# Kernel optimization log

Hardware: AMD Instinct MI355X
Metric: run time of the kernel (lower is better)

## Reference

```python
import jax, jax.numpy as jnp
from jax import lax
import numpy as np

B, C, L, H, W = 2, 64, 16, 64, 64
K = 7
NG = 4  # GroupNorm groups (SpatialGroupNorm(4, channels))


def setup_inputs() -> dict:
    key = jax.random.key(0)
    ks = jax.random.split(key, 16)
    s = lambda i, shape, sc: jax.random.normal(ks[i], shape, jnp.float32) * sc
    return {
        "x": s(0, (B, C, L, H, W), 1.0),
        "dt": jax.random.uniform(ks[1], (B, L), jnp.float32, 0.1, 1.0),
        "W_sp": s(2, (C, C, K, K), 0.02),      # spatial 7x7 conv (OIHW)
        "W_dc": s(3, (C, C), 0.1),             # 1x1x1 depth conv
        "b_dc": jnp.zeros((C,), jnp.float32),
        "gn_g": jnp.ones((C,), jnp.float32),
        "gn_b": jnp.zeros((C,), jnp.float32),
        "W_in": s(4, (2 * C, C), 0.1),         # pw_conv_in 1x1 -> 2C (gated)
        "b_in": jnp.zeros((2 * C,), jnp.float32),
        "W_out": s(5, (C, C), 0.1),            # pw_conv_out 1x1
        "b_out": jnp.zeros((C,), jnp.float32),
        "nu_log": s(6, (C,), 0.5),             # LRU log decay rate
        "theta_log": s(7, (C,), 0.5),          # LRU log frequency
        "c_re": s(8, (C,), 0.5),               # LRU output mix (real)
        "c_im": s(9, (C,), 0.5),               # LRU output mix (imag)
        "d_skip": s(10, (C,), 0.5),            # LRU feedthrough
    }


def reference(x, dt, W_sp, W_dc, b_dc, gn_g, gn_b, W_in, b_in, W_out, b_out,
              nu_log, theta_log, c_re, c_im, d_skip):
    Bb, Cc, Ll, Hh, Ww = x.shape
    pad = W_sp.shape[-1] // 2
    # --- GatedConvBlock: FactorizedPeriodicConv3d (per-frame 2D conv) ---
    xf = x.transpose(0, 2, 1, 3, 4).reshape(Bb * Ll, Cc, Hh, Ww)  # [B*L,C,H,W]
    xp = jnp.pad(xf, ((0, 0), (0, 0), (0, 0), (pad, pad)), mode='wrap')    # circular W
    xp = jnp.pad(xp, ((0, 0), (0, 0), (pad, pad), (0, 0)), mode='edge')    # replicate H
    y = lax.conv_general_dilated(xp, W_sp, (1, 1), 'VALID',
                                 dimension_numbers=('NCHW', 'OIHW', 'NCHW'))
    y = jnp.einsum('nchw,oc->nohw', y, W_dc) + b_dc[None, :, None, None]   # depth 1x1x1
    # --- SpatialGroupNorm (per frame, 4 groups) ---
    g = y.reshape(Bb * Ll, NG, Cc // NG, Hh, Ww)
    mu = g.mean(axis=(2, 3, 4), keepdims=True)
    var = g.var(axis=(2, 3, 4), keepdims=True)
    y = ((g - mu) * lax.rsqrt(var + 1e-5)).reshape(Bb * Ll, Cc, Hh, Ww)
    y = y * gn_g[None, :, None, None] + gn_b[None, :, None, None]
    # --- gated pointwise convs + residual ---
    h = jnp.einsum('nchw,oc->nohw', y, W_in) + b_in[None, :, None, None]
    x1, x2 = jnp.split(h, 2, axis=1)
    z = x1 * jax.nn.sigmoid(x2)
    z = jnp.einsum('nchw,oc->nohw', z, W_out) + b_out[None, :, None, None]
    u = xf + z                                     # residual, [B*L,C,H,W]
    u = u.reshape(Bb, Ll, Cc, Hh, Ww).transpose(1, 0, 2, 3, 4)  # [L,B,C,H,W]
    # --- LRU: dt-dependent complex diagonal recurrence over L ---
    decay = jnp.exp(-jnp.exp(nu_log)[None, None, :] * dt[:, :, None])   # [B,L,C]
    phase = jnp.exp(theta_log)[None, None, :] * dt[:, :, None]          # [B,L,C]
    lam_re = (decay * jnp.cos(phase)).transpose(1, 0, 2)[..., None, None]  # [L,B,C,1,1]
    lam_im = (decay * jnp.sin(phase)).transpose(1, 0, 2)[..., None, None]
    gamma = jnp.sqrt(jnp.maximum(1.0 - decay ** 2, 1e-6)).transpose(1, 0, 2)[..., None, None]
    cr = c_re[None, :, None, None]
    ci = c_im[None, :, None, None]
    ds = d_skip[None, :, None, None]

    def step(carry, inputs):
        h_re, h_im = carry
        ut, lr, li, gm = inputs
        nr = lr * h_re - li * h_im + gm * ut
        ni = li * h_re + lr * h_im
        yt = cr * nr + ci * ni + ds * ut
        return (nr, ni), yt

    init = (jnp.zeros((Bb, Cc, Hh, Ww), x.dtype), jnp.zeros((Bb, Cc, Hh, Ww), x.dtype))
    _, ys = lax.scan(step, init, (u, lam_re, lam_im, gamma))   # ys: [L,B,C,H,W]
    return ys.transpose(1, 2, 0, 3, 4)                         # [B,C,L,H,W]
```

## Files before the change

### kernel.cpp

```cpp
#include <hip/hip_runtime.h>
#include <hip/hip_bf16.h>

typedef short bf16x8 __attribute__((ext_vector_type(8)));
typedef float f32x16 __attribute__((ext_vector_type(16)));

#define B_ 2
#define C_ 64
#define L_ 16
#define N_ 32
#define HW_ 4096

#define BY_WPH  0u
#define BY_WP1  401408u
#define BY_WP2  434176u
#define BY_OFF1 450560u
#define BY_LR   451072u
#define BY_LI   459264u
#define BY_GM   467456u
#define BY_PART 475648u
#define BY_XHI  524288u
#define BY_U    524288u

__device__ __forceinline__ unsigned short f2bf(float v) {
    unsigned int u = __float_as_uint(v);
    unsigned int r = u + 0x7FFFu + ((u >> 16) & 1u);
    return (unsigned short)(r >> 16);
}
__device__ __forceinline__ float bf2f(unsigned short s) {
    return __uint_as_float(((unsigned int)s) << 16);
}

__global__ void k_setup(const float* __restrict__ W_sp, const float* __restrict__ W_dc,
                        unsigned short* __restrict__ WpH,
                        const float* __restrict__ W_in, const float* __restrict__ b_in,
                        const float* __restrict__ W_out,
                        const float* __restrict__ gn_g, const float* __restrict__ gn_b,
                        unsigned short* __restrict__ WP1, unsigned short* __restrict__ WP2,
                        float* __restrict__ OFF1,
                        const float* __restrict__ dt, const float* __restrict__ nu_log,
                        const float* __restrict__ theta_log,
                        float* __restrict__ lr_t, float* __restrict__ li_t,
                        float* __restrict__ gm_t) {
    int blk = blockIdx.x, tid = threadIdx.x;
    if (blk < 98) {
        int idx = blk * 256 + tid;
        if (idx >= 49 * 512) return;
        int lane = idx & 63;
        int ks   = (idx >> 6) & 3;
        int nf   = (idx >> 8) & 1;
        int tap  = idx >> 9;
        int oc   = nf * 32 + (lane & 31);
        int icb  = ks * 16 + (lane >> 5) * 8;
        unsigned short h8[8];
        #pragma unroll
        for (int e = 0; e < 8; ++e) {
            int ic = icb + e;
            float s = 0.f;
            for (int c = 0; c < 64; ++c)
                s += W_dc[oc * 64 + c] * W_sp[(c * 64 + ic) * 49 + tap];
            h8[e] = f2bf(s);
        }
        #pragma unroll
        for (int e = 0; e < 8; ++e) WpH[idx * 8 + e] = h8[e];
    } else if (blk < 111) {
        int idx = (blk - 98) * 256 + tid;
        if (idx < 2048) {
            int lane = idx & 63, ks = (idx >> 6) & 3, nf = (idx >> 8) & 3, hl = idx >> 10;
            int o = nf * 32 + (lane & 31), cb = ks * 16 + (lane >> 5) * 8;
            #pragma unroll
            for (int e = 0; e < 8; ++e) {
                float v = W_in[o * 64 + cb + e] * gn_g[cb + e];
                unsigned short h = f2bf(v);
                WP1[idx * 8 + e] = hl ? f2bf(v - bf2f(h)) : h;
            }
        } else if (idx < 3072) {
            int i2 = idx - 2048;
            int lane = i2 & 63, ks = (i2 >> 6) & 3, nf = (i2 >> 8) & 1, hl = i2 >> 9;
            int j = nf * 32 + (lane & 31), ob = ks * 16 + (lane >> 5) * 8;
            #pragma unroll
            for (int e = 0; e < 8; ++e) {
                float v = W_out[j * 64 + ob + e];
                unsigned short h = f2bf(v);
                WP2[i2 * 8 + e] = hl ? f2bf(v - bf2f(h)) : h;
            }
        } else if (idx < 3200) {
            int o = idx - 3072;
            float s = b_in[o];
            for (int c = 0; c < 64; ++c) s += W_in[o * 64 + c] * gn_b[c];
            OFF1[o] = s;
        }
    } else {
        int idx = (blk - 111) * 256 + tid;
        if (idx >= N_ * C_) return;
        int c = idx & 63, n = idx >> 6;
        float dtv = dt[n];
        float decay = expf(-expf(nu_log[c]) * dtv);
        float phase = expf(theta_log[c]) * dtv;
        lr_t[idx] = decay * cosf(phase);
        li_t[idx] = decay * sinf(phase);
        gm_t[idx] = sqrtf(fmaxf(1.f - decay * decay, 1e-6f));
    }
}

__global__ __launch_bounds__(256) void k_tr(const float* __restrict__ x,
                                            unsigned short* __restrict__ xhi) {
    __shared__ float t[64][129];
    int blk = blockIdx.x;
    int n = blk >> 5, seg = blk & 31;
    int p0 = seg * 128;
    int b = n >> 4, l = n & 15;
    int tid = threadIdx.x;
    for (int i = 0; i < 32; ++i) {
        int idx = i * 256 + tid;
        int ic = idx >> 7, p = idx & 127;
        t[ic][p] = x[(((size_t)(b * 64 + ic) * 16 + l)) * 4096 + p0 + p];
    }
    __syncthreads();
    for (int it = 0; it < 4; ++it) {
        int chunk = it * 256 + tid;
        int p = chunk >> 3, c0 = (chunk & 7) * 8;
        unsigned short h8[8];
        #pragma unroll
        for (int e = 0; e < 8; ++e) h8[e] = f2bf(t[c0 + e][p]);
        size_t off = ((size_t)(n * 4096 + p0 + p)) * 64 + c0;
        *(uint4*)&xhi[off] = *(uint4*)h8;
    }
}

__global__ __launch_bounds__(256, 2) void k_conv(
    const unsigned short* __restrict__ xhi,
    const unsigned short* __restrict__ WpH,
    const float* __restrict__ b_dc, float* __restrict__ y,
    float* __restrict__ part) {
    __shared__ uint4 halo[3904];
    __shared__ float ps[4][8], pq[4][8];
    int tid = threadIdx.x;
    int tile = blockIdx.x;
    int th = tile >> 2, tw = tile & 3;
    int n = blockIdx.y;
    int lane = tid & 63, wid = tid >> 6;
    int dh = (lane >> 4) & 1, dw = lane & 15, kslot = lane >> 5;

    for (int u2 = wid; u2 < 61; u2 += 4) {
        int row = u2 * 8 + (lane >> 3);
        if (row > 483) row = 483;
        int hh = row / 22, ww = row - hh * 22;
        int hs = th * 16 + hh - 3; hs = hs < 0 ? 0 : (hs > 63 ? 63 : hs);
        int wv = (tw * 16 + ww - 3) & 63;
        const uint4* src = (const uint4*)(xhi + ((size_t)n * 4096 + hs * 64 + wv) * 64) + (lane & 7);
        uint4 v = *src;
        *(uint4*)((char*)halo + ((row << 7) + (((lane & 7) ^ (row & 7)) << 4))) = v;
    }
    __syncthreads();

    f32x16 acc[2][2] = {};
    bf16x8 Aa[2][4], Ab[2][4], Ba[2][4], Bb[2][4];

#define LOADA(Areg, khv, kwv) { \
    _Pragma("unroll") for (int m = 0; m < 2; ++m) { \
        int rowb = (wid * 4 + 2 * m + dh + (khv)) * 22 + dw + (kwv); \
        _Pragma("unroll") for (int ks = 0; ks < 4; ++ks) { \
            int byt = (rowb << 7) + (((2 * ks + kslot) ^ (rowb & 7)) << 4); \
            Areg[m][ks] = *(const bf16x8*)((const char*)halo + byt); } } }

#define LOADB(Breg, tap) { \
    const bf16x8* WH = (const bf16x8*)WpH + (size_t)(tap) * 512 + lane; \
    _Pragma("unroll") for (int nf = 0; nf < 2; ++nf) \
        _Pragma("unroll") for (int ks = 0; ks < 4; ++ks) \
            Breg[nf][ks] = WH[(nf * 4 + ks) * 64]; }

#define MFMA_ALL(Areg, Breg) { \
    _Pragma("unroll") for (int ks = 0; ks < 4; ++ks) \
        _Pragma("unroll") for (int m = 0; m < 2; ++m) \
            _Pragma("unroll") for (int nf = 0; nf < 2; ++nf) \
                acc[m][nf] = __builtin_amdgcn_mfma_f32_32x32x16_bf16(Areg[m][ks], Breg[nf][ks], acc[m][nf], 0, 0, 0); }

    int kh = 0, kw = 0;
    LOADA(Aa, 0, 0); LOADB(Ba, 0);
    for (int t = 0; t < 48; t += 2) {
        ++kw; if (kw == 7) { kw = 0; ++kh; }
        LOADA(Ab, kh, kw);
        MFMA_ALL(Aa, Ba);
        LOADB(Bb, t + 1);
        ++kw; if (kw == 7) { kw = 0; ++kh; }
        LOADA(Aa, kh, kw);
        MFMA_ALL(Ab, Bb);
        LOADB(Ba, t + 2);
    }
    MFMA_ALL(Aa, Ba);
#undef LOADA
#undef LOADB
#undef MFMA_ALL

    int ocl = lane & 31;
    float sg[2], qg[2];
    #pragma unroll
    for (int nf = 0; nf < 2; ++nf) {
        float bv = b_dc[nf * 32 + ocl];
        float ss = 0.f, qq = 0.f;
        #pragma unroll
        for (int m = 0; m < 2; ++m) {
            #pragma unroll
            for (int j = 0; j < 16; ++j) {
                int r = (j & 3) + 8 * (j >> 2) + 4 * (lane >> 5);
                int h = th * 16 + wid * 4 + 2 * m + (r >> 4);
                int w = tw * 16 + (r & 15);
                float v = acc[m][nf][j] + bv;
                y[((size_t)n * 4096 + h * 64 + w) * 64 + nf * 32 + ocl] = v;
                ss += v; qq += v * v;
            }
        }
        sg[nf] = ss; qg[nf] = qq;
    }
    #pragma unroll
    for (int off = 1; off < 16; off <<= 1) {
        sg[0] += __shfl_xor(sg[0], off);
        qg[0] += __shfl_xor(qg[0], off);
        sg[1] += __shfl_xor(sg[1], off);
        qg[1] += __shfl_xor(qg[1], off);
    }
    if ((lane & 15) == 0) {
        int cl = lane >> 4;
        int g0 = cl & 1, slot = wid * 2 + (cl >> 1);
        ps[g0][slot] = sg[0];     pq[g0][slot] = qg[0];
        ps[2 + g0][slot] = sg[1]; pq[2 + g0][slot] = qg[1];
    }
    __syncthreads();
    if (tid < 4) {
        float ss = 0.f, qq = 0.f;
        #pragma unroll
        for (int k2 = 0; k2 < 8; ++k2) { ss += ps[tid][k2]; qq += pq[tid][k2]; }
        part[((size_t)(n * 16 + tile)) * 8 + tid * 2]     = ss;
        part[((size_t)(n * 16 + tile)) * 8 + tid * 2 + 1] = qq;
    }
}

__global__ __launch_bounds__(256, 1) void k_pw(
    const float* __restrict__ y, const float* __restrict__ part,
    const unsigned short* __restrict__ WP1, const unsigned short* __restrict__ WP2,
    const float* __restrict__ OFF1, const float* __restrict__ b_out,
    const float* __restrict__ x, float* __restrict__ u) {
    __shared__ __align__(16) char lds[4 * 8704];
    int tid = threadIdx.x, lane = tid & 63, wid = tid >> 6;
    int blk = blockIdx.x;
    int n = blk >> 5, sub = blk & 31;
    int b = n >> 4, l = n & 15;
    int ocl = lane & 31, hi5 = lane >> 5;
    int pixw = sub * 128 + wid * 32;
    char* myl = lds + wid * 8704;

    float mu[4], rsd[4];
    #pragma unroll
    for (int g = 0; g < 4; ++g) {
        float sm = 0.f, sq = 0.f;
        #pragma unroll
        for (int ch = 0; ch < 16; ++ch) {
            sm += part[(n * 16 + ch) * 8 + g * 2];
            sq += part[(n * 16 + ch) * 8 + g * 2 + 1];
        }
        float mean = sm * (1.f / 65536.f);
        float var  = sq * (1.f / 65536.f) - mean * mean;
        mu[g] = mean;
        rsd[g] = rsqrtf(var + 1e-5f);
    }

    const bf16x8* W1 = (const bf16x8*)WP1;
    const bf16x8* W2 = (const bf16x8*)WP2;

    int prow = pixw + ocl;

    bf16x8 A1[4];
    #pragma unroll
    for (int ks = 0; ks < 4; ++ks) {
        const float* yb = &y[(size_t)(n * 4096 + prow) * 64 + ks * 16 + hi5 * 8];
        float4 va = *(const float4*)yb;
        float4 vb = *(const float4*)(yb + 4);
        float m = mu[ks], r = rsd[ks];
        bf16x8 a;
        a[0] = (short)f2bf((va.x - m) * r); a[1] = (short)f2bf((va.y - m) * r);
        a[2] = (short)f2bf((va.z - m) * r); a[3] = (short)f2bf((va.w - m) * r);
        a[4] = (short)f2bf((vb.x - m) * r); a[5] = (short)f2bf((vb.y - m) * r);
        a[6] = (short)f2bf((vb.z - m) * r); a[7] = (short)f2bf((vb.w - m) * r);
        A1[ks] = a;
    }

    f32x16 acc1[4];
    #pragma unroll
    for (int nf = 0; nf < 4; ++nf) {
        float o0 = OFF1[nf * 32 + ocl];
        #pragma unroll
        for (int j = 0; j < 16; ++j) acc1[nf][j] = o0;
    }
    #pragma unroll
    for (int ks = 0; ks < 4; ++ks)
        #pragma unroll
        for (int nf = 0; nf < 4; ++nf) {
            bf16x8 bh = W1[nf * 256 + ks * 64 + lane];
            bf16x8 bl = W1[1024 + nf * 256 + ks * 64 + lane];
            acc1[nf] = __builtin_amdgcn_mfma_f32_32x32x16_bf16(A1[ks], bh, acc1[nf], 0, 0, 0);
            acc1[nf] = __builtin_amdgcn_mfma_f32_32x32x16_bf16(A1[ks], bl, acc1[nf], 0, 0, 0);
        }

    unsigned short* zp = (unsigned short*)myl;
    #pragma unroll
    for (int nf = 0; nf < 2; ++nf)
        #pragma unroll
        for (int j = 0; j < 16; ++j) {
            int r = (j & 3) + 8 * (j >> 2) + 4 * hi5;
            float x1 = acc1[nf][j], x2 = acc1[nf + 2][j];
            float z = x1 / (1.f + __expf(-x2));
            zp[r * 68 + nf * 32 + ocl] = f2bf(z);
        }
    asm volatile("s_waitcnt lgkmcnt(0)" ::: "memory");
    __builtin_amdgcn_sched_barrier(0);

    bf16x8 A2[4];
    #pragma unroll
    for (int ks = 0; ks < 4; ++ks)
        A2[ks] = *(const bf16x8*)(myl + ocl * 136 + ks * 32 + hi5 * 16);

    f32x16 acc2[2];
    #pragma unroll
    for (int nf = 0; nf < 2; ++nf)
        #pragma unroll
        for (int j = 0; j < 16; ++j) acc2[nf][j] = 0.f;
    #pragma unroll
    for (int ks = 0; ks < 4; ++ks)
        #pragma unroll
        for (int nf = 0; nf < 2; ++nf) {
            bf16x8 bh = W2[nf * 256 + ks * 64 + lane];
            bf16x8 bl = W2[512 + nf * 256 + ks * 64 + lane];
            acc2[nf] = __builtin_amdgcn_mfma_f32_32x32x16_bf16(A2[ks], bh, acc2[nf], 0, 0, 0);
            acc2[nf] = __builtin_amdgcn_mfma_f32_32x32x16_bf16(A2[ks], bl, acc2[nf], 0, 0, 0);
        }
    asm volatile("s_waitcnt lgkmcnt(0)" ::: "memory");
    __builtin_amdgcn_sched_barrier(0);

    float* up = (float*)myl;
    #pragma unroll
    for (int nf = 0; nf < 2; ++nf)
        #pragma unroll
        for (int j = 0; j < 16; ++j) {
            int r = (j & 3) + 8 * (j >> 2) + 4 * hi5;
            up[r * 68 + nf * 32 + ocl] = acc2[nf][j];
        }
    asm volatile("s_waitcnt lgkmcnt(0)" ::: "memory");
    __builtin_amdgcn_sched_barrier(0);

    {
        float* rowp = up + ocl * 68 + hi5 * 32;
        float vrow[32];
        #pragma unroll
        for (int c4 = 0; c4 < 8; ++c4) {
            float4 v = *(const float4*)&rowp[c4 * 4];
            vrow[c4 * 4 + 0] = v.x; vrow[c4 * 4 + 1] = v.y;
            vrow[c4 * 4 + 2] = v.z; vrow[c4 * 4 + 3] = v.w;
        }
        int pixg = pixw + ocl;
        #pragma unroll
        for (int k = 0; k < 32; ++k) {
            int c = hi5 * 32 + k;
            vrow[k] += b_out[c] + x[((size_t)(b * 64 + c) * 16 + l) * 4096 + pixg];
        }
        #pragma unroll
        for (int c4 = 0; c4 < 8; ++c4) {
            float4 v;
            v.x = vrow[c4 * 4 + 0]; v.y = vrow[c4 * 4 + 1];
            v.z = vrow[c4 * 4 + 2]; v.w = vrow[c4 * 4 + 3];
            *(float4*)&rowp[c4 * 4] = v;
        }
    }
    asm volatile("s_waitcnt lgkmcnt(0)" ::: "memory");
    __builtin_amdgcn_sched_barrier(0);

    #pragma unroll
    for (int i = 0; i < 8; ++i) {
        int e = i * 64 + lane;
        int row = e >> 4, c4 = e & 15;
        float4 v = *(const float4*)&up[row * 68 + c4 * 4];
        *(float4*)&u[((size_t)(n * 4096 + pixw + row)) * 64 + c4 * 4] = v;
    }
    asm volatile("s_waitcnt lgkmcnt(0)" ::: "memory");
    __builtin_amdgcn_sched_barrier(0);
}

__global__ __launch_bounds__(256) void k_scan(
    const float* __restrict__ u, const float* __restrict__ lr_t,
    const float* __restrict__ li_t, const float* __restrict__ gm_t,
    const float* __restrict__ c_re, const float* __restrict__ c_im,
    const float* __restrict__ d_skip, float* __restrict__ out) {
    __shared__ float us[16][68];
    int tid = threadIdx.x;
    int bid = blockIdx.x;
    int b = bid >> 8, h = (bid >> 2) & 63, wq = bid & 3;
    int c4 = tid & 15, p = tid >> 4;
    int w = wq * 16 + p;
    float4 cr4 = *(const float4*)&c_re[c4 * 4];
    float4 ci4 = *(const float4*)&c_im[c4 * 4];
    float4 ds4 = *(const float4*)&d_skip[c4 * 4];
    float hr[4] = {}, hi[4] = {};
    int wp = tid & 15, cc = tid >> 4;
    for (int l = 0; l < 16; ++l) {
        int n = b * 16 + l;
        float4 uv = *(const float4*)&u[((size_t)(n * 4096 + h * 64 + w)) * 64 + c4 * 4];
        float4 lr4 = *(const float4*)&lr_t[n * 64 + c4 * 4];
        float4 li4 = *(const float4*)&li_t[n * 64 + c4 * 4];
        float4 gm4 = *(const float4*)&gm_t[n * 64 + c4 * 4];
        float yv[4];
        {
            float ut = uv.x, lr = lr4.x, li = li4.x;
            float nr = lr * hr[0] - li * hi[0] + gm4.x * ut;
            float ni = li * hr[0] + lr * hi[0];
            yv[0] = cr4.x * nr + ci4.x * ni + ds4.x * ut; hr[0] = nr; hi[0] = ni;
        }
        {
            float ut = uv.y, lr = lr4.y, li = li4.y;
            float nr = lr * hr[1] - li * hi[1] + gm4.y * ut;
            float ni = li * hr[1] + lr * hi[1];
            yv[1] = cr4.y * nr + ci4.y * ni + ds4.y * ut; hr[1] = nr; hi[1] = ni;
        }
        {
            float ut = uv.z, lr = lr4.z, li = li4.z;
            float nr = lr * hr[2] - li * hi[2] + gm4.z * ut;
            float ni = li * hr[2] + lr * hi[2];
            yv[2] = cr4.z * nr + ci4.z * ni + ds4.z * ut; hr[2] = nr; hi[2] = ni;
        }
        {
            float ut = uv.w, lr = lr4.w, li = li4.w;
            float nr = lr * hr[3] - li * hi[3] + gm4.w * ut;
            float ni = li * hr[3] + lr * hi[3];
            yv[3] = cr4.w * nr + ci4.w * ni + ds4.w * ut; hr[3] = nr; hi[3] = ni;
        }
        *(float4*)&us[p][c4 * 4] = *(float4*)yv;
        __syncthreads();
        #pragma unroll
        for (int j = 0; j < 4; ++j) {
            int c = cc * 4 + j;
            out[((size_t)(b * 64 + c) * 16 + l) * 4096 + h * 64 + wq * 16 + wp] = us[wp][c];
        }
        __syncthreads();
    }
}

extern "C" void kernel_launch(void* const* d_in, const int* in_sizes, int n_in,
                              void* d_out, int out_size, void* d_ws, size_t ws_size,
                              hipStream_t stream) {
    const float* x        = (const float*)d_in[0];
    const float* dt       = (const float*)d_in[1];
    const float* W_sp     = (const float*)d_in[2];
    const float* W_dc     = (const float*)d_in[3];
    const float* b_dc     = (const float*)d_in[4];
    const float* gn_g     = (const float*)d_in[5];
    const float* gn_b     = (const float*)d_in[6];
    const float* W_in     = (const float*)d_in[7];
    const float* b_in     = (const float*)d_in[8];
    const float* W_out    = (const float*)d_in[9];
    const float* b_out    = (const float*)d_in[10];
    const float* nu_log   = (const float*)d_in[11];
    const float* theta_log= (const float*)d_in[12];
    const float* c_re     = (const float*)d_in[13];
    const float* c_im     = (const float*)d_in[14];
    const float* d_skip   = (const float*)d_in[15];

    char* ws = (char*)d_ws;
    unsigned short* WpH  = (unsigned short*)(ws + BY_WPH);
    unsigned short* WP1  = (unsigned short*)(ws + BY_WP1);
    unsigned short* WP2  = (unsigned short*)(ws + BY_WP2);
    float* OFF1   = (float*)(ws + BY_OFF1);
    float* lr_t   = (float*)(ws + BY_LR);
    float* li_t   = (float*)(ws + BY_LI);
    float* gm_t   = (float*)(ws + BY_GM);
    float* part   = (float*)(ws + BY_PART);
    unsigned short* xhi = (unsigned short*)(ws + BY_XHI);
    float* u      = (float*)(ws + BY_U);
    float* y      = (float*)d_out;
    float* out    = (float*)d_out;

    hipLaunchKernelGGL(k_setup,   dim3(119),       dim3(256), 0, stream,
                       W_sp, W_dc, WpH, W_in, b_in, W_out, gn_g, gn_b, WP1, WP2, OFF1,
                       dt, nu_log, theta_log, lr_t, li_t, gm_t);
    hipLaunchKernelGGL(k_tr,      dim3(1024),      dim3(256), 0, stream, x, xhi);
    hipLaunchKernelGGL(k_conv,    dim3(16, 32),    dim3(256), 0, stream, xhi, WpH, b_dc, y, part);
    hipLaunchKernelGGL(k_pw,      dim3(1024),      dim3(256), 0, stream, y, part, WP1, WP2,
                       OFF1, b_out, x, u);
    hipLaunchKernelGGL(k_scan,    dim3(512),       dim3(256), 0, stream, u, lr_t, li_t, gm_t,
                       c_re, c_im, d_skip, out);
}
```

Baseline: 134.7 us.

## Store conv output as bf16, add MFMA priority hints, restructure scan kernel

The conv intermediate y is now written and read as bf16 instead of fp32, halving that round-trip through memory. GroupNorm statistics are still taken from fp32 values, but normalization reads the rounded values, which adds a small precision loss. s_setprio hints are placed around the MFMA blocks in k_conv and k_pw. The scan kernel is split into twice as many blocks, each handling 32 channels, with next-step loads prefetched and a double-buffered LDS tile that removes one barrier per step.

```diff
diff --git a/kernel.cpp b/kernel.cpp
--- a/kernel.cpp
+++ b/kernel.cpp
@@ -130,7 +130,7 @@
 __global__ __launch_bounds__(256, 2) void k_conv(
     const unsigned short* __restrict__ xhi,
     const unsigned short* __restrict__ WpH,
-    const float* __restrict__ b_dc, float* __restrict__ y,
+    const float* __restrict__ b_dc, unsigned short* __restrict__ y,
     float* __restrict__ part) {
     __shared__ uint4 halo[3904];
     __shared__ float ps[4][8], pq[4][8];
@@ -170,10 +170,12 @@
             Breg[nf][ks] = WH[(nf * 4 + ks) * 64]; }
 
 #define MFMA_ALL(Areg, Breg) { \
+    __builtin_amdgcn_s_setprio(1); \
     _Pragma("unroll") for (int ks = 0; ks < 4; ++ks) \
         _Pragma("unroll") for (int m = 0; m < 2; ++m) \
             _Pragma("unroll") for (int nf = 0; nf < 2; ++nf) \
-                acc[m][nf] = __builtin_amdgcn_mfma_f32_32x32x16_bf16(Areg[m][ks], Breg[nf][ks], acc[m][nf], 0, 0, 0); }
+                acc[m][nf] = __builtin_amdgcn_mfma_f32_32x32x16_bf16(Areg[m][ks], Breg[nf][ks], acc[m][nf], 0, 0, 0); \
+    __builtin_amdgcn_s_setprio(0); }
 
     int kh = 0, kw = 0;
     LOADA(Aa, 0, 0); LOADB(Ba, 0);
@@ -206,7 +208,7 @@
                 int h = th * 16 + wid * 4 + 2 * m + (r >> 4);
                 int w = tw * 16 + (r & 15);
                 float v = acc[m][nf][j] + bv;
-                y[((size_t)n * 4096 + h * 64 + w) * 64 + nf * 32 + ocl] = v;
+                y[((size_t)n * 4096 + h * 64 + w) * 64 + nf * 32 + ocl] = f2bf(v);
                 ss += v; qq += v * v;
             }
         }
@@ -236,7 +238,7 @@
 }
 
 __global__ __launch_bounds__(256, 1) void k_pw(
-    const float* __restrict__ y, const float* __restrict__ part,
+    const unsigned short* __restrict__ y, const float* __restrict__ part,
     const unsigned short* __restrict__ WP1, const unsigned short* __restrict__ WP2,
     const float* __restrict__ OFF1, const float* __restrict__ b_out,
     const float* __restrict__ x, float* __restrict__ u) {
@@ -272,15 +274,12 @@
     bf16x8 A1[4];
     #pragma unroll
     for (int ks = 0; ks < 4; ++ks) {
-        const float* yb = &y[(size_t)(n * 4096 + prow) * 64 + ks * 16 + hi5 * 8];
-        float4 va = *(const float4*)yb;
-        float4 vb = *(const float4*)(yb + 4);
+        bf16x8 raw = *(const bf16x8*)&y[(size_t)(n * 4096 + prow) * 64 + ks * 16 + hi5 * 8];
         float m = mu[ks], r = rsd[ks];
         bf16x8 a;
-        a[0] = (short)f2bf((va.x - m) * r); a[1] = (short)f2bf((va.y - m) * r);
-        a[2] = (short)f2bf((va.z - m) * r); a[3] = (short)f2bf((va.w - m) * r);
-        a[4] = (short)f2bf((vb.x - m) * r); a[5] = (short)f2bf((vb.y - m) * r);
-        a[6] = (short)f2bf((vb.z - m) * r); a[7] = (short)f2bf((vb.w - m) * r);
+        #pragma unroll
+        for (int e = 0; e < 8; ++e)
+            a[e] = (short)f2bf((bf2f((unsigned short)raw[e]) - m) * r);
         A1[ks] = a;
     }
 
@@ -291,6 +290,7 @@
         #pragma unroll
         for (int j = 0; j < 16; ++j) acc1[nf][j] = o0;
     }
+    __builtin_amdgcn_s_setprio(1);
     #pragma unroll
     for (int ks = 0; ks < 4; ++ks)
         #pragma unroll
@@ -300,6 +300,7 @@
             acc1[nf] = __builtin_amdgcn_mfma_f32_32x32x16_bf16(A1[ks], bh, acc1[nf], 0, 0, 0);
             acc1[nf] = __builtin_amdgcn_mfma_f32_32x32x16_bf16(A1[ks], bl, acc1[nf], 0, 0, 0);
         }
+    __builtin_amdgcn_s_setprio(0);
 
     unsigned short* zp = (unsigned short*)myl;
     #pragma unroll
@@ -324,6 +325,7 @@
     for (int nf = 0; nf < 2; ++nf)
         #pragma unroll
         for (int j = 0; j < 16; ++j) acc2[nf][j] = 0.f;
+    __builtin_amdgcn_s_setprio(1);
     #pragma unroll
     for (int ks = 0; ks < 4; ++ks)
         #pragma unroll
@@ -333,6 +335,7 @@
             acc2[nf] = __builtin_amdgcn_mfma_f32_32x32x16_bf16(A2[ks], bh, acc2[nf], 0, 0, 0);
             acc2[nf] = __builtin_amdgcn_mfma_f32_32x32x16_bf16(A2[ks], bl, acc2[nf], 0, 0, 0);
         }
+    __builtin_amdgcn_s_setprio(0);
     asm volatile("s_waitcnt lgkmcnt(0)" ::: "memory");
     __builtin_amdgcn_sched_barrier(0);
 
@@ -389,56 +392,44 @@
     const float* __restrict__ li_t, const float* __restrict__ gm_t,
     const float* __restrict__ c_re, const float* __restrict__ c_im,
     const float* __restrict__ d_skip, float* __restrict__ out) {
-    __shared__ float us[16][68];
+    __shared__ float us[2][16][36];
     int tid = threadIdx.x;
     int bid = blockIdx.x;
-    int b = bid >> 8, h = (bid >> 2) & 63, wq = bid & 3;
-    int c4 = tid & 15, p = tid >> 4;
+    int b = bid >> 9, h = (bid >> 3) & 63, wq = (bid >> 1) & 3, ch = bid & 1;
+    int c2 = tid & 15, p = tid >> 4;
     int w = wq * 16 + p;
-    float4 cr4 = *(const float4*)&c_re[c4 * 4];
-    float4 ci4 = *(const float4*)&c_im[c4 * 4];
-    float4 ds4 = *(const float4*)&d_skip[c4 * 4];
-    float hr[4] = {}, hi[4] = {};
+    int cbase = ch * 32 + c2 * 2;
+    float2 cr2 = *(const float2*)&c_re[cbase];
+    float2 ci2 = *(const float2*)&c_im[cbase];
+    float2 ds2 = *(const float2*)&d_skip[cbase];
+    float hr0 = 0.f, hi0 = 0.f, hr1 = 0.f, hi1 = 0.f;
     int wp = tid & 15, cc = tid >> 4;
+    size_t ubase = ((size_t)(b * 16) * 4096 + h * 64 + w) * 64 + cbase;
+    int lbase = (b * 16) * 64 + cbase;
+    float2 uv  = *(const float2*)&u[ubase];
+    float2 lr2 = *(const float2*)&lr_t[lbase];
+    float2 li2 = *(const float2*)&li_t[lbase];
+    float2 gm2 = *(const float2*)&gm_t[lbase];
     for (int l = 0; l < 16; ++l) {
-        int n = b * 16 + l;
-        float4 uv = *(const float4*)&u[((size_t)(n * 4096 + h * 64 + w)) * 64 + c4 * 4];
-        float4 lr4 = *(const float4*)&lr_t[n * 64 + c4 * 4];
-        float4 li4 = *(const float4*)&li_t[n * 64 + c4 * 4];
-        float4 gm4 = *(const float4*)&gm_t[n * 64 + c4 * 4];
-        float yv[4];
-        {
-            float ut = uv.x, lr = lr4.x, li = li4.x;
-            float nr = lr * hr[0] - li * hi[0] + gm4.x * ut;
-            float ni = li * hr[0] + lr * hi[0];
-            yv[0] = cr4.x * nr + ci4.x * ni + ds4.x * ut; hr[0] = nr; hi[0] = ni;
-        }
-        {
-            float ut = uv.y, lr = lr4.y, li = li4.y;
-            float nr = lr * hr[1] - li * hi[1] + gm4.y * ut;
-            float ni = li * hr[1] + lr * hi[1];
-            yv[1] = cr4.y * nr + ci4.y * ni + ds4.y * ut; hr[1] = nr; hi[1] = ni;
-        }
-        {
-            float ut = uv.z, lr = lr4.z, li = li4.z;
-            float nr = lr * hr[2] - li * hi[2] + gm4.z * ut;
-            float ni = li * hr[2] + lr * hi[2];
-            yv[2] = cr4.z * nr + ci4.z * ni + ds4.z * ut; hr[2] = nr; hi[2] = ni;
-        }
-        {
-            float ut = uv.w, lr = lr4.w, li = li4.w;
-            float nr = lr * hr[3] - li * hi[3] + gm4.w * ut;
-            float ni = li * hr[3] + lr * hi[3];
-            yv[3] = cr4.w * nr + ci4.w * ni + ds4.w * ut; hr[3] = nr; hi[3] = ni;
-        }
-        *(float4*)&us[p][c4 * 4] = *(float4*)yv;
+        float2 uvn, lrn, lin, gmn;
+        if (l < 15) {
+            uvn = *(const float2*)&u[ubase + (size_t)(l + 1) * 262144];
+            lrn = *(const float2*)&lr_t[lbase + (l + 1) * 64];
+            lin = *(const float2*)&li_t[lbase + (l + 1) * 64];
+            gmn = *(const float2*)&gm_t[lbase + (l + 1) * 64];
+        }
+        float nr0 = lr2.x * hr0 - li2.x * hi0 + gm2.x * uv.x;
+        float ni0 = li2.x * hr0 + lr2.x * hi0;
+        float y0  = cr2.x * nr0 + ci2.x * ni0 + ds2.x * uv.x; hr0 = nr0; hi0 = ni0;
+        float nr1 = lr2.y * hr1 - li2.y * hi1 + gm2.y * uv.y;
+        float ni1 = li2.y * hr1 + lr2.y * hi1;
+        float y1  = cr2.y * nr1 + ci2.y * ni1 + ds2.y * uv.y; hr1 = nr1; hi1 = ni1;
+        float2 st; st.x = y0; st.y = y1;
+        *(float2*)&us[l & 1][p][c2 * 2] = st;
         __syncthreads();
-        #pragma unroll
-        for (int j = 0; j < 4; ++j) {
-            int c = cc * 4 + j;
-            out[((size_t)(b * 64 + c) * 16 + l) * 4096 + h * 64 + wq * 16 + wp] = us[wp][c];
-        }
-        __syncthreads();
+        out[((size_t)(b * 64 + ch * 32 + cc * 2)     * 16 + l) * 4096 + h * 64 + wq * 16 + wp] = us[l & 1][wp][cc * 2];
+        out[((size_t)(b * 64 + ch * 32 + cc * 2 + 1) * 16 + l) * 4096 + h * 64 + wq * 16 + wp] = us[l & 1][wp][cc * 2 + 1];
+        uv = uvn; lr2 = lrn; li2 = lin; gm2 = gmn;
     }
 }
 
@@ -473,16 +464,16 @@
     float* part   = (float*)(ws + BY_PART);
     unsigned short* xhi = (unsigned short*)(ws + BY_XHI);
     float* u      = (float*)(ws + BY_U);
-    float* y      = (float*)d_out;
+    unsigned short* y16 = (unsigned short*)d_out;
     float* out    = (float*)d_out;
 
     hipLaunchKernelGGL(k_setup,   dim3(119),       dim3(256), 0, stream,
                        W_sp, W_dc, WpH, W_in, b_in, W_out, gn_g, gn_b, WP1, WP2, OFF1,
                        dt, nu_log, theta_log, lr_t, li_t, gm_t);
     hipLaunchKernelGGL(k_tr,      dim3(1024),      dim3(256), 0, stream, x, xhi);
-    hipLaunchKernelGGL(k_conv,    dim3(16, 32),    dim3(256), 0, stream, xhi, WpH, b_dc, y, part);
-    hipLaunchKernelGGL(k_pw,      dim3(1024),      dim3(256), 0, stream, y, part, WP1, WP2,
+    hipLaunchKernelGGL(k_conv,    dim3(16, 32),    dim3(256), 0, stream, xhi, WpH, b_dc, y16, part);
+    hipLaunchKernelGGL(k_pw,      dim3(1024),      dim3(256), 0, stream, y16, part, WP1, WP2,
                        OFF1, b_out, x, u);
-    hipLaunchKernelGGL(k_scan,    dim3(512),       dim3(256), 0, stream, u, lr_t, li_t, gm_t,
+    hipLaunchKernelGGL(k_scan,    dim3(1024),      dim3(256), 0, stream, u, lr_t, li_t, gm_t,
                        c_re, c_im, d_skip, out);
 }
```

New measurement: 134.7 us. Within noise of the previous version (+0.0%).
